# Kernel tuning notes

Measured on AMD Instinct MI355X. Metric: run time of the kernel, lower is better.

Reference implementation:

```python
import jax, jax.numpy as jnp
import numpy as np

B, S, F, H = 16, 2048, 1024, 16
D = F // H
EPS = 1e-5


def setup_inputs() -> dict:
    key = jax.random.key(0)
    ks = jax.random.split(key, 10)
    scale = 1.0 / np.sqrt(F)
    return {
        "x": jax.random.normal(ks[0], (B, S, F), jnp.float32),
        "Wq": jax.random.normal(ks[1], (F, F), jnp.float32) * scale,
        "bq": jnp.zeros((F,), jnp.float32),
        "Wk": jax.random.normal(ks[2], (F, F), jnp.float32) * scale,
        "bk": jnp.zeros((F,), jnp.float32),
        "Wv": jax.random.normal(ks[3], (F, F), jnp.float32) * scale,
        "bv": jnp.zeros((F,), jnp.float32),
        "Wo": jax.random.normal(ks[4], (F, F), jnp.float32) * scale,
        "bo": jnp.zeros((F,), jnp.float32),
        "gamma": jnp.ones((F,), jnp.float32),
        "beta": jnp.zeros((F,), jnp.float32),
    }


def reference(x, Wq, bq, Wk, bk, Wv, bv, Wo, bo, gamma, beta):
    # x: (B, S, F). Dropout is identity in eval mode.
    b, s, f = x.shape
    q = (x @ Wq + bq).reshape(b, s, H, D)
    k = (x @ Wk + bk).reshape(b, s, H, D)
    v = (x @ Wv + bv).reshape(b, s, H, D)
    # Faithful to source: the einsum (applied to permuted tensors) contracts
    # across HEADS at each sequence position -> scores (B, S, H, H).
    energy = jnp.einsum('bshd,bsgd->bshg', q, k) / (D ** 0.5)
    attn = jax.nn.softmax(energy, axis=-1)  # softmax over key-head axis
    out = jnp.einsum('bshg,bsgd->bshd', attn, v).reshape(b, s, f)
    out = out @ Wo + bo
    # LayerNorm over last dim (eps=1e-5, affine)
    mu = jnp.mean(out, axis=-1, keepdims=True)
    var = jnp.mean((out - mu) ** 2, axis=-1, keepdims=True)
    return (out - mu) * jax.lax.rsqrt(var + EPS) * gamma + beta
```

## Files before the change

### kernel.cpp

```cpp
#include <hip/hip_runtime.h>
#include <hip/hip_bf16.h>
#include <stdint.h>

#define MM   32768
#define FFD  1024
#define NQKV 3072

typedef __bf16 bf16x8 __attribute__((ext_vector_type(8)));
typedef float  f32x4  __attribute__((ext_vector_type(4)));

__device__ __forceinline__ unsigned short f2bf_bits(float f){
  __hip_bfloat16 h = __float2bfloat16(f);
  unsigned short u;
  __builtin_memcpy(&u, &h, 2);
  return u;
}

__device__ __forceinline__ void gld16(const void* g, void* l){
  const unsigned int* gu = (const unsigned int*)g;
  unsigned int* lu = (unsigned int*)l;
  __builtin_amdgcn_global_load_lds(
      (const __attribute__((address_space(1))) unsigned int*)gu,
      (__attribute__((address_space(3))) unsigned int*)lu,
      16, 0, 0);
}

#define BARRIER() do { asm volatile("" ::: "memory"); \
                       __builtin_amdgcn_s_barrier();  \
                       asm volatile("" ::: "memory"); } while(0)

__global__ __launch_bounds__(256) void k_convert_bf16(const float* __restrict__ in,
                                                      unsigned short* __restrict__ out,
                                                      int n4){
  int i = blockIdx.x * 256 + threadIdx.x;
  if (i >= n4) return;
  float4 v = ((const float4*)in)[i];
  ushort4 r;
  r.x = f2bf_bits(v.x); r.y = f2bf_bits(v.y);
  r.z = f2bf_bits(v.z); r.w = f2bf_bits(v.w);
  ((ushort4*)out)[i] = r;
}

__global__ __launch_bounds__(256) void k_transpose_bf16(const float* __restrict__ in,
                                                        unsigned short* __restrict__ out,
                                                        int rows, int cols){
  __shared__ float tile[32][33];
  int bc = blockIdx.x * 32, br = blockIdx.y * 32;
  int tx = threadIdx.x, ty = threadIdx.y;
  #pragma unroll
  for (int j = 0; j < 32; j += 8)
    tile[ty + j][tx] = in[(size_t)(br + ty + j) * cols + bc + tx];
  __syncthreads();
  #pragma unroll
  for (int j = 0; j < 32; j += 8)
    out[(size_t)(bc + ty + j) * rows + br + tx] = f2bf_bits(tile[tx][ty + j]);
}

template <bool BF16OUT>
__global__ __launch_bounds__(512, 2) void k_gemm_bt(
    const unsigned short* __restrict__ A,
    const unsigned short* __restrict__ Bt,
    const float* __restrict__ b0, const float* __restrict__ b1, const float* __restrict__ b2,
    void* __restrict__ Cout, int M, int N, int K)
{
  __shared__ alignas(16) char smem[131072];

  const int tid  = threadIdx.x;
  const int lane = tid & 63;
  const int wave = tid >> 6;
  const int wr = wave >> 2, wc = wave & 3;
  const int quad = lane >> 4, lrow = lane & 15;
  const int sa = ((lrow >> 1) & 3) << 4;

  const int nwgx = gridDim.x;
  int nwg = nwgx * gridDim.y;
  int bid = blockIdx.y * nwgx + blockIdx.x;
  int cpx = nwg >> 3;
  int nid = (bid & 7) * cpx + (bid >> 3);
  int by = nid / nwgx;
  int bx = nid - by * nwgx;

  const long rowBase = (long)by * 256;
  const long colBase = (long)bx * 256;

  f32x4 acc[8][4];
  #pragma unroll
  for (int i = 0; i < 8; i++)
    #pragma unroll
    for (int j = 0; j < 4; j++)
      acc[i][j] = (f32x4){0.f, 0.f, 0.f, 0.f};

  const int swz8 = 8 * ((tid & 3) ^ ((tid >> 3) & 3));
  const unsigned short* gA = A  + (rowBase + (tid >> 2)) * (long)K + swz8;
  const unsigned short* gB = Bt + (colBase + (tid >> 2)) * (long)K + swz8;
  const long hstep = 128L * K;

  const int nk = K >> 5;

  #pragma unroll
  for (int tt = 0; tt < 3; ++tt){
    char* nb = smem + tt * 32768;
    gld16(gA + tt * 32,         nb +         tid * 16);
    gld16(gA + tt * 32 + hstep, nb +  8192 + tid * 16);
    gld16(gB + tt * 32,         nb + 16384 + tid * 16);
    gld16(gB + tt * 32 + hstep, nb + 24576 + tid * 16);
  }

  for (int t = 0; t < nk; ++t){
    if (t <= nk - 3)      asm volatile("s_waitcnt vmcnt(8)" ::: "memory");
    else if (t == nk - 2) asm volatile("s_waitcnt vmcnt(4)" ::: "memory");
    else                  asm volatile("s_waitcnt vmcnt(0)" ::: "memory");
    BARRIER();

    char* buf = smem + (t & 3) * 32768;
    if (t < nk - 3){
      char* nb = smem + ((t + 3) & 3) * 32768;
      const unsigned short* sA = gA + (long)(t + 3) * 32;
      const unsigned short* sB = gB + (long)(t + 3) * 32;
      gld16(sA,         nb +         tid * 16);
      gld16(sA + hstep, nb +  8192 + tid * 16);
      gld16(sB,         nb + 16384 + tid * 16);
      gld16(sB + 24576 / 16 * 0 + hstep, nb + 24576 + tid * 16);
    }

    bf16x8 bfr[4];
    const char* bb = buf + 16384 + wc * 4096 + lrow * 64 + ((quad * 16) ^ sa);
    #pragma unroll
    for (int n = 0; n < 4; ++n)
      bfr[n] = *(const bf16x8*)(bb + n * 1024);

    #pragma unroll
    for (int p = 0; p < 2; ++p){
      bf16x8 af[4];
      const char* ab = buf + wr * 8192 + p * 4096 + lrow * 64 + ((quad * 16) ^ sa);
      #pragma unroll
      for (int f = 0; f < 4; ++f)
        af[f] = *(const bf16x8*)(ab + f * 1024);
      __builtin_amdgcn_s_setprio(1);
      #pragma unroll
      for (int f = 0; f < 4; ++f)
        #pragma unroll
        for (int n = 0; n < 4; ++n)
          acc[p * 4 + f][n] =
              __builtin_amdgcn_mfma_f32_16x16x32_bf16(af[f], bfr[n], acc[p * 4 + f][n], 0, 0, 0);
      __builtin_amdgcn_s_setprio(0);
    }
  }

  if constexpr (BF16OUT){
    BARRIER();
    #pragma unroll
    for (int n = 0; n < 4; ++n){
      int lcol = wc * 64 + n * 16 + lrow;
      long col = colBase + lcol;
      const float* bp = (col < 1024) ? b0 : ((col < 2048) ? b1 : b2);
      float bias = bp[col & 1023];
      #pragma unroll
      for (int m = 0; m < 8; ++m){
        int row0 = wr * 128 + (m >> 2) * 64 + (m & 3) * 16 + quad * 4;
        int sw = ((row0 >> 2) & 3) << 5;
        #pragma unroll
        for (int r = 0; r < 4; ++r){
          float v = acc[m][n][r] + bias;
          int byte = (row0 + r) * 512 + ((lcol * 2) ^ sw);
          *(unsigned short*)(smem + byte) = f2bf_bits(v);
        }
      }
    }
    asm volatile("s_waitcnt lgkmcnt(0)" ::: "memory");
    BARRIER();
    unsigned short* Cо = (unsigned short*)Cout;
    #pragma unroll
    for (int i = 0; i < 16; ++i){
      int c = i * 512 + tid;
      int row = c >> 5, cidx = c & 31;
      int rb = (cidx ^ (((row >> 2) & 3) << 1)) * 16;
      uint4 u = *(const uint4*)(smem + row * 512 + rb);
      *(uint4*)(Cо + (rowBase + row) * (long)N + colBase + cidx * 8) = u;
    }
  } else {
    #pragma unroll
    for (int n = 0; n < 4; ++n){
      long col = colBase + wc * 64 + n * 16 + lrow;
      const float* bp = (col < 1024) ? b0 : ((col < 2048) ? b1 : b2);
      float bias = bp[col & 1023];
      #pragma unroll
      for (int m = 0; m < 8; ++m){
        long row0 = rowBase + wr * 128 + (m >> 2) * 64 + (m & 3) * 16 + quad * 4;
        #pragma unroll
        for (int r = 0; r < 4; ++r){
          float v = acc[m][n][r] + bias;
          ((float*)Cout)[(row0 + r) * (long)N + col] = v;
        }
      }
    }
  }
}

__global__ __launch_bounds__(256) void k_attention(const unsigned short* __restrict__ qkv,
                                                   unsigned short* __restrict__ aout){
  constexpr int QOFF = 0;
  constexpr int KOFF = 1152;
  constexpr int VOFF = 2304;
  constexpr int POFF = 4864;
  constexpr int PER  = 5504;
  __shared__ unsigned short smem[4 * PER];

  const int lane = threadIdx.x & 63;
  const int wave = threadIdx.x >> 6;
  const int pos  = blockIdx.x * 4 + wave;
  const int quad = lane >> 4, lidx = lane & 15;

  unsigned short* base = smem + wave * PER;
  unsigned short* Qb = base + QOFF;
  unsigned short* Kb = base + KOFF;
  unsigned short* Vt = base + VOFF;
  unsigned short* Pb = base + POFF;

  {
    uint4 z = {0u, 0u, 0u, 0u};
    *(uint4*)(Vt + lane * 40 + 16) = z;
    *(uint4*)(Vt + lane * 40 + 24) = z;
    *(uint2*)(Pb + (lane >> 2) * 40 + 16 + (lane & 3) * 4) = make_uint2(0u, 0u);
  }

  const unsigned short* src = qkv + (size_t)pos * 3072;
  #pragma unroll
  for (int i = 0; i < 6; i++){
    int c = i * 64 + lane;
    uint4 u = *(const uint4*)(src + c * 8);
    if (i < 4){
      unsigned short* mb = (c < 128) ? Qb : Kb;
      int cc = c & 127;
      *(uint4*)(mb + (cc >> 3) * 72 + (cc & 7) * 8) = u;
    } else {
      int cv = c - 256;
      int g = cv >> 3, d0 = (cv & 7) * 8;
      const unsigned short* us = (const unsigned short*)&u;
      #pragma unroll
      for (int t = 0; t < 8; t++) Vt[(d0 + t) * 40 + g] = us[t];
    }
  }
  __syncthreads();

  f32x4 s = (f32x4){0.f, 0.f, 0.f, 0.f};
  #pragma unroll
  for (int kk = 0; kk < 2; kk++){
    bf16x8 a = *(const bf16x8*)(Qb + lidx * 72 + kk * 32 + quad * 8);
    bf16x8 b = *(const bf16x8*)(Kb + lidx * 72 + kk * 32 + quad * 8);
    s = __builtin_amdgcn_mfma_f32_16x16x32_bf16(a, b, s, 0, 0, 0);
  }

  #pragma unroll
  for (int r = 0; r < 4; r++){
    float v = s[r] * 0.125f;
    float m = v;
    m = fmaxf(m, __shfl_xor(m, 1));
    m = fmaxf(m, __shfl_xor(m, 2));
    m = fmaxf(m, __shfl_xor(m, 4));
    m = fmaxf(m, __shfl_xor(m, 8));
    float e = __expf(v - m);
    float sum = e;
    sum += __shfl_xor(sum, 1);
    sum += __shfl_xor(sum, 2);
    sum += __shfl_xor(sum, 4);
    sum += __shfl_xor(sum, 8);
    float p = e / sum;
    Pb[(quad * 4 + r) * 40 + lidx] = f2bf_bits(p);
  }
  __syncthreads();

  f32x4 o[4];
  #pragma unroll
  for (int n4 = 0; n4 < 4; n4++){
    bf16x8 a = *(const bf16x8*)(Pb + lidx * 40 + quad * 8);
    bf16x8 b = *(const bf16x8*)(Vt + (n4 * 16 + lidx) * 40 + quad * 8);
    o[n4] = __builtin_amdgcn_mfma_f32_16x16x32_bf16(a, b, (f32x4){0.f,0.f,0.f,0.f}, 0, 0, 0);
  }

  #pragma unroll
  for (int n4 = 0; n4 < 4; n4++)
    #pragma unroll
    for (int r = 0; r < 4; r++)
      Qb[(quad * 4 + r) * 72 + n4 * 16 + lidx] = f2bf_bits(o[n4][r]);
  __syncthreads();

  unsigned short* dst = aout + (size_t)pos * 1024;
  #pragma unroll
  for (int t = 0; t < 2; t++){
    int j = lane * 2 + t;
    int h = j >> 3, dc = j & 7;
    uint4 u = *(const uint4*)(Qb + h * 72 + dc * 8);
    *(uint4*)(dst + j * 8) = u;
  }
}

__global__ __launch_bounds__(256) void k_ln(float* __restrict__ out,
                                            const float* __restrict__ gamma,
                                            const float* __restrict__ beta){
  __shared__ float red[8];
  int tid = threadIdx.x;
  float4* rowp = (float4*)(out + (size_t)blockIdx.x * 1024);
  float4 v = rowp[tid];
  float s  = v.x + v.y + v.z + v.w;
  float ss = v.x * v.x + v.y * v.y + v.z * v.z + v.w * v.w;
  #pragma unroll
  for (int off = 32; off > 0; off >>= 1){
    s  += __shfl_down(s, off);
    ss += __shfl_down(ss, off);
  }
  if ((tid & 63) == 0){ red[tid >> 6] = s; red[4 + (tid >> 6)] = ss; }
  __syncthreads();
  float S  = red[0] + red[1] + red[2] + red[3];
  float SS = red[4] + red[5] + red[6] + red[7];
  float mean = S * (1.0f / 1024.0f);
  float var  = SS * (1.0f / 1024.0f) - mean * mean;
  float rstd = rsqrtf(var + 1e-5f);
  float4 g = ((const float4*)gamma)[tid];
  float4 b = ((const float4*)beta)[tid];
  v.x = (v.x - mean) * rstd * g.x + b.x;
  v.y = (v.y - mean) * rstd * g.y + b.y;
  v.z = (v.z - mean) * rstd * g.z + b.z;
  v.w = (v.w - mean) * rstd * g.w + b.w;
  rowp[tid] = v;
}

extern "C" void kernel_launch(void* const* d_in, const int* in_sizes, int n_in,
                              void* d_out, int out_size, void* d_ws, size_t ws_size,
                              hipStream_t stream){
  const float* x     = (const float*)d_in[0];
  const float* Wq    = (const float*)d_in[1];
  const float* bq    = (const float*)d_in[2];
  const float* Wk    = (const float*)d_in[3];
  const float* bk    = (const float*)d_in[4];
  const float* Wv    = (const float*)d_in[5];
  const float* bv    = (const float*)d_in[6];
  const float* Wo    = (const float*)d_in[7];
  const float* bo    = (const float*)d_in[8];
  const float* gamma = (const float*)d_in[9];
  const float* beta  = (const float*)d_in[10];
  float* out = (float*)d_out;

  char* ws = (char*)d_ws;
  unsigned short* Wqkv_t = (unsigned short*)ws;
  unsigned short* Wo_t   = (unsigned short*)(ws + 6291456);
  unsigned short* xb     = (unsigned short*)(ws + 8388608);
  unsigned short* qkv    = (unsigned short*)(ws + 75497472);
  unsigned short* aout   = xb;

  k_convert_bf16<<<32768, 256, 0, stream>>>(x, xb, (MM * FFD) / 4);

  dim3 tb(32, 8), tg(32, 32);
  k_transpose_bf16<<<tg, tb, 0, stream>>>(Wq, Wqkv_t,                1024, 1024);
  k_transpose_bf16<<<tg, tb, 0, stream>>>(Wk, Wqkv_t + 1024 * 1024,  1024, 1024);
  k_transpose_bf16<<<tg, tb, 0, stream>>>(Wv, Wqkv_t + 2048 * 1024,  1024, 1024);
  k_transpose_bf16<<<tg, tb, 0, stream>>>(Wo, Wo_t,                  1024, 1024);

  k_gemm_bt<true><<<dim3(NQKV / 256, MM / 256), 512, 0, stream>>>(
      xb, Wqkv_t, bq, bk, bv, qkv, MM, NQKV, FFD);

  k_attention<<<MM / 4, 256, 0, stream>>>(qkv, aout);

  k_gemm_bt<false><<<dim3(FFD / 256, MM / 256), 512, 0, stream>>>(
      aout, Wo_t, bo, bo, bo, out, MM, FFD, FFD);

  k_ln<<<MM, 256, 0, stream>>>(out, gamma, beta);
}
```

Measured before the change: 631.0 us.

## Interleave global-to-LDS prefetch with MFMA phases using explicit barriers

The GEMM main loop is restructured into two phases per K-step. Each phase loads the A fragments from LDS, then issues half of the next-stage global-to-LDS prefetch (A halves first, B halves second), then a workgroup barrier, an LDS wait and a scheduling fence before a block of MFMAs at raised priority. The aim is to spread the memory issue between compute blocks so loads and matrix ops from different waves overlap better, ping-pong style. The cost is two or three extra workgroup barriers per iteration, which may stall waves and reduce overlap. A variable name containing a non-ASCII character is also renamed.

```diff
diff --git a/kernel.cpp b/kernel.cpp
--- a/kernel.cpp
+++ b/kernel.cpp
@@ -113,38 +113,54 @@
     BARRIER();
 
     char* buf = smem + (t & 3) * 32768;
-    if (t < nk - 3){
-      char* nb = smem + ((t + 3) & 3) * 32768;
-      const unsigned short* sA = gA + (long)(t + 3) * 32;
-      const unsigned short* sB = gB + (long)(t + 3) * 32;
-      gld16(sA,         nb +         tid * 16);
-      gld16(sA + hstep, nb +  8192 + tid * 16);
-      gld16(sB,         nb + 16384 + tid * 16);
-      gld16(sB + 24576 / 16 * 0 + hstep, nb + 24576 + tid * 16);
-    }
-
-    bf16x8 bfr[4];
+    char* nb  = smem + ((t + 3) & 3) * 32768;
+    const bool st = (t < nk - 3);
+    const unsigned short* sA = gA + (long)(t + 3) * 32;
+    const unsigned short* sB = gB + (long)(t + 3) * 32;
+
+    bf16x8 bfr[4], af[4];
     const char* bb = buf + 16384 + wc * 4096 + lrow * 64 + ((quad * 16) ^ sa);
     #pragma unroll
     for (int n = 0; n < 4; ++n)
       bfr[n] = *(const bf16x8*)(bb + n * 1024);
-
-    #pragma unroll
-    for (int p = 0; p < 2; ++p){
-      bf16x8 af[4];
-      const char* ab = buf + wr * 8192 + p * 4096 + lrow * 64 + ((quad * 16) ^ sa);
-      #pragma unroll
-      for (int f = 0; f < 4; ++f)
-        af[f] = *(const bf16x8*)(ab + f * 1024);
-      __builtin_amdgcn_s_setprio(1);
-      #pragma unroll
-      for (int f = 0; f < 4; ++f)
-        #pragma unroll
-        for (int n = 0; n < 4; ++n)
-          acc[p * 4 + f][n] =
-              __builtin_amdgcn_mfma_f32_16x16x32_bf16(af[f], bfr[n], acc[p * 4 + f][n], 0, 0, 0);
-      __builtin_amdgcn_s_setprio(0);
-    }
+    const char* ab0 = buf + wr * 8192 + lrow * 64 + ((quad * 16) ^ sa);
+    #pragma unroll
+    for (int f = 0; f < 4; ++f)
+      af[f] = *(const bf16x8*)(ab0 + f * 1024);
+    if (st){
+      gld16(sA,         nb +        tid * 16);
+      gld16(sA + hstep, nb + 8192 + tid * 16);
+    }
+    BARRIER();
+    asm volatile("s_waitcnt lgkmcnt(0)" ::: "memory");
+    __builtin_amdgcn_sched_barrier(0);
+    __builtin_amdgcn_s_setprio(1);
+    #pragma unroll
+    for (int f = 0; f < 4; ++f)
+      #pragma unroll
+      for (int n = 0; n < 4; ++n)
+        acc[f][n] = __builtin_amdgcn_mfma_f32_16x16x32_bf16(af[f], bfr[n], acc[f][n], 0, 0, 0);
+    __builtin_amdgcn_s_setprio(0);
+    BARRIER();
+
+    const char* ab1 = buf + wr * 8192 + 4096 + lrow * 64 + ((quad * 16) ^ sa);
+    #pragma unroll
+    for (int f = 0; f < 4; ++f)
+      af[f] = *(const bf16x8*)(ab1 + f * 1024);
+    if (st){
+      gld16(sB,         nb + 16384 + tid * 16);
+      gld16(sB + hstep, nb + 24576 + tid * 16);
+    }
+    BARRIER();
+    asm volatile("s_waitcnt lgkmcnt(0)" ::: "memory");
+    __builtin_amdgcn_sched_barrier(0);
+    __builtin_amdgcn_s_setprio(1);
+    #pragma unroll
+    for (int f = 0; f < 4; ++f)
+      #pragma unroll
+      for (int n = 0; n < 4; ++n)
+        acc[4 + f][n] = __builtin_amdgcn_mfma_f32_16x16x32_bf16(af[f], bfr[n], acc[4 + f][n], 0, 0, 0);
+    __builtin_amdgcn_s_setprio(0);
   }
 
   if constexpr (BF16OUT){
@@ -169,14 +185,14 @@
     }
     asm volatile("s_waitcnt lgkmcnt(0)" ::: "memory");
     BARRIER();
-    unsigned short* Cо = (unsigned short*)Cout;
+    unsigned short* Cb = (unsigned short*)Cout;
     #pragma unroll
     for (int i = 0; i < 16; ++i){
       int c = i * 512 + tid;
       int row = c >> 5, cidx = c & 31;
       int rb = (cidx ^ (((row >> 2) & 3) << 1)) * 16;
       uint4 u = *(const uint4*)(smem + row * 512 + rb);
-      *(uint4*)(Cо + (rowBase + row) * (long)N + colBase + cidx * 8) = u;
+      *(uint4*)(Cb + (rowBase + row) * (long)N + colBase + cidx * 8) = u;
     }
   } else {
     #pragma unroll
```

Result: no change. 626.8 us (-0.7%).

## Rewrite head-attention kernel to load operands directly from global, drop LDS staging

Applied to the files above, without the earlier changes.

The per-position attention kernel no longer stages Q, K, V and P through shared memory with several __syncthreads. It loads MFMA operands straight from global memory, computes the transposed score matrix so softmax reduces with cross-quad shuffles, builds the P operand via lane shuffles, and gathers V elements per lane before the second MFMA. Results are written straight to global. This removes LDS traffic, block-level barriers and the shared allocation, at the cost of scattered 2-byte global loads for V and some shuffle overhead. It also renames a variable that used a non-ASCII character and cleans up a redundant expression.

```diff
diff --git a/kernel.cpp b/kernel.cpp
--- a/kernel.cpp
+++ b/kernel.cpp
@@ -120,7 +120,7 @@
       gld16(sA,         nb +         tid * 16);
       gld16(sA + hstep, nb +  8192 + tid * 16);
       gld16(sB,         nb + 16384 + tid * 16);
-      gld16(sB + 24576 / 16 * 0 + hstep, nb + 24576 + tid * 16);
+      gld16(sB + hstep, nb + 24576 + tid * 16);
     }
 
     bf16x8 bfr[4];
@@ -169,14 +169,14 @@
     }
     asm volatile("s_waitcnt lgkmcnt(0)" ::: "memory");
     BARRIER();
-    unsigned short* Cо = (unsigned short*)Cout;
+    unsigned short* Cb = (unsigned short*)Cout;
     #pragma unroll
     for (int i = 0; i < 16; ++i){
       int c = i * 512 + tid;
       int row = c >> 5, cidx = c & 31;
       int rb = (cidx ^ (((row >> 2) & 3) << 1)) * 16;
       uint4 u = *(const uint4*)(smem + row * 512 + rb);
-      *(uint4*)(Cо + (rowBase + row) * (long)N + colBase + cidx * 8) = u;
+      *(uint4*)(Cb + (rowBase + row) * (long)N + colBase + cidx * 8) = u;
     }
   } else {
     #pragma unroll
@@ -199,99 +199,61 @@
 
 __global__ __launch_bounds__(256) void k_attention(const unsigned short* __restrict__ qkv,
                                                    unsigned short* __restrict__ aout){
-  constexpr int QOFF = 0;
-  constexpr int KOFF = 1152;
-  constexpr int VOFF = 2304;
-  constexpr int POFF = 4864;
-  constexpr int PER  = 5504;
-  __shared__ unsigned short smem[4 * PER];
-
   const int lane = threadIdx.x & 63;
   const int wave = threadIdx.x >> 6;
   const int pos  = blockIdx.x * 4 + wave;
   const int quad = lane >> 4, lidx = lane & 15;
 
-  unsigned short* base = smem + wave * PER;
-  unsigned short* Qb = base + QOFF;
-  unsigned short* Kb = base + KOFF;
-  unsigned short* Vt = base + VOFF;
-  unsigned short* Pb = base + POFF;
-
-  {
-    uint4 z = {0u, 0u, 0u, 0u};
-    *(uint4*)(Vt + lane * 40 + 16) = z;
-    *(uint4*)(Vt + lane * 40 + 24) = z;
-    *(uint2*)(Pb + (lane >> 2) * 40 + 16 + (lane & 3) * 4) = make_uint2(0u, 0u);
-  }
-
   const unsigned short* src = qkv + (size_t)pos * 3072;
-  #pragma unroll
-  for (int i = 0; i < 6; i++){
-    int c = i * 64 + lane;
-    uint4 u = *(const uint4*)(src + c * 8);
-    if (i < 4){
-      unsigned short* mb = (c < 128) ? Qb : Kb;
-      int cc = c & 127;
-      *(uint4*)(mb + (cc >> 3) * 72 + (cc & 7) * 8) = u;
-    } else {
-      int cv = c - 256;
-      int g = cv >> 3, d0 = (cv & 7) * 8;
-      const unsigned short* us = (const unsigned short*)&u;
-      #pragma unroll
-      for (int t = 0; t < 8; t++) Vt[(d0 + t) * 40 + g] = us[t];
-    }
-  }
-  __syncthreads();
 
   f32x4 s = (f32x4){0.f, 0.f, 0.f, 0.f};
   #pragma unroll
-  for (int kk = 0; kk < 2; kk++){
-    bf16x8 a = *(const bf16x8*)(Qb + lidx * 72 + kk * 32 + quad * 8);
-    bf16x8 b = *(const bf16x8*)(Kb + lidx * 72 + kk * 32 + quad * 8);
-    s = __builtin_amdgcn_mfma_f32_16x16x32_bf16(a, b, s, 0, 0, 0);
-  }
-
-  #pragma unroll
-  for (int r = 0; r < 4; r++){
-    float v = s[r] * 0.125f;
-    float m = v;
-    m = fmaxf(m, __shfl_xor(m, 1));
-    m = fmaxf(m, __shfl_xor(m, 2));
-    m = fmaxf(m, __shfl_xor(m, 4));
-    m = fmaxf(m, __shfl_xor(m, 8));
-    float e = __expf(v - m);
-    float sum = e;
-    sum += __shfl_xor(sum, 1);
-    sum += __shfl_xor(sum, 2);
-    sum += __shfl_xor(sum, 4);
-    sum += __shfl_xor(sum, 8);
-    float p = e / sum;
-    Pb[(quad * 4 + r) * 40 + lidx] = f2bf_bits(p);
-  }
-  __syncthreads();
-
-  f32x4 o[4];
-  #pragma unroll
-  for (int n4 = 0; n4 < 4; n4++){
-    bf16x8 a = *(const bf16x8*)(Pb + lidx * 40 + quad * 8);
-    bf16x8 b = *(const bf16x8*)(Vt + (n4 * 16 + lidx) * 40 + quad * 8);
-    o[n4] = __builtin_amdgcn_mfma_f32_16x16x32_bf16(a, b, (f32x4){0.f,0.f,0.f,0.f}, 0, 0, 0);
-  }
-
-  #pragma unroll
-  for (int n4 = 0; n4 < 4; n4++)
-    #pragma unroll
-    for (int r = 0; r < 4; r++)
-      Qb[(quad * 4 + r) * 72 + n4 * 16 + lidx] = f2bf_bits(o[n4][r]);
-  __syncthreads();
-
+  for (int kk = 0; kk < 2; ++kk){
+    bf16x8 aK = *(const bf16x8*)(src + 1024 + lidx * 64 + kk * 32 + quad * 8);
+    bf16x8 bQ = *(const bf16x8*)(src +        lidx * 64 + kk * 32 + quad * 8);
+    s = __builtin_amdgcn_mfma_f32_16x16x32_bf16(aK, bQ, s, 0, 0, 0);
+  }
+
+  float v0 = s[0] * 0.125f, v1 = s[1] * 0.125f;
+  float v2 = s[2] * 0.125f, v3 = s[3] * 0.125f;
+  float m = fmaxf(fmaxf(v0, v1), fmaxf(v2, v3));
+  m = fmaxf(m, __shfl_xor(m, 16));
+  m = fmaxf(m, __shfl_xor(m, 32));
+  float e0 = __expf(v0 - m), e1 = __expf(v1 - m);
+  float e2 = __expf(v2 - m), e3 = __expf(v3 - m);
+  float sum = e0 + e1 + e2 + e3;
+  sum += __shfl_xor(sum, 16);
+  sum += __shfl_xor(sum, 32);
+  float inv = 1.0f / sum;
+  unsigned P01 = (unsigned)f2bf_bits(e0 * inv) | ((unsigned)f2bf_bits(e1 * inv) << 16);
+  unsigned P23 = (unsigned)f2bf_bits(e2 * inv) | ((unsigned)f2bf_bits(e3 * inv) << 16);
+
+  int sA = ((quad * 32) + lidx) & 63;
+  int sB = (sA + 16) & 63;
+  unsigned w0 = (unsigned)__shfl((int)P01, sA);
+  unsigned w1 = (unsigned)__shfl((int)P23, sA);
+  unsigned w2 = (unsigned)__shfl((int)P01, sB);
+  unsigned w3 = (unsigned)__shfl((int)P23, sB);
+  if (quad >= 2){ w0 = 0u; w1 = 0u; w2 = 0u; w3 = 0u; }
+  union { unsigned u[4]; bf16x8 v; } bp;
+  bp.u[0] = w0; bp.u[1] = w1; bp.u[2] = w2; bp.u[3] = w3;
+
+  const unsigned short* Vp = src + 2048;
   unsigned short* dst = aout + (size_t)pos * 1024;
   #pragma unroll
-  for (int t = 0; t < 2; t++){
-    int j = lane * 2 + t;
-    int h = j >> 3, dc = j & 7;
-    uint4 u = *(const uint4*)(Qb + h * 72 + dc * 8);
-    *(uint4*)(dst + j * 8) = u;
+  for (int n4 = 0; n4 < 4; ++n4){
+    union { unsigned short us[8]; bf16x8 v; } av;
+    #pragma unroll
+    for (int j = 0; j < 8; ++j){
+      unsigned short rv = Vp[((quad * 8 + j) & 15) * 64 + n4 * 16 + lidx];
+      av.us[j] = (quad < 2) ? rv : (unsigned short)0;
+    }
+    f32x4 o = __builtin_amdgcn_mfma_f32_16x16x32_bf16(
+        av.v, bp.v, (f32x4){0.f, 0.f, 0.f, 0.f}, 0, 0, 0);
+    unsigned lo = (unsigned)f2bf_bits(o[0]) | ((unsigned)f2bf_bits(o[1]) << 16);
+    unsigned hi = (unsigned)f2bf_bits(o[2]) | ((unsigned)f2bf_bits(o[3]) << 16);
+    uint2 st; st.x = lo; st.y = hi;
+    *(uint2*)(dst + lidx * 64 + n4 * 16 + quad * 4) = st;
   }
 }
 
```

After: 643.9 us. +2.0%, slower.
